# Kernel tuning notes

Hardware: AMD Instinct MI355X
Metric: run time of the kernel (lower is better)

Reference implementation:

```python
import jax, jax.numpy as jnp
import numpy as np

B, T, D, H = 64, 512, 256, 1024


def setup_inputs() -> dict:
    key = jax.random.key(0)
    ks = jax.random.split(key, 4)
    def xavier(k, shape):
        fan_in, fan_out = shape[1], shape[0]
        lim = np.sqrt(6.0 / (fan_in + fan_out)).astype(np.float32)
        return jax.random.uniform(k, shape, jnp.float32, -lim, lim)
    inputs = jax.random.normal(ks[0], (B, T, D), dtype=jnp.float32)
    Wx = xavier(ks[1], (4 * H, D))      # x2h weight
    bx = jnp.zeros((4 * H,), jnp.float32)
    Wh = xavier(ks[2], (4 * H, H))      # h2h weight
    bh = jnp.zeros((4 * H,), jnp.float32)
    Wout = xavier(ks[3], (D, H))        # output head
    bout = jnp.zeros((D,), jnp.float32)
    return {"inputs": inputs, "Wx": Wx, "bx": bx, "Wh": Wh, "bh": bh,
            "Wout": Wout, "bout": bout}


def _lstm_seq(inputs, Wx, bx, Wh, bh):
    # Precompute input-to-hidden gates for all timesteps: (T, B, 4H)
    xg = jnp.einsum('btd,gd->tbg', inputs, Wx) + bx
    h0 = jnp.zeros((inputs.shape[0], H), inputs.dtype)
    c0 = jnp.zeros_like(h0)

    def step(carry, xg_t):
        h, c = carry
        gates = xg_t + h @ Wh.T + bh            # (B, 4H)
        i, f, g, o = jnp.split(jax.nn.sigmoid(gates), 4, axis=-1)
        # NOTE: source applies sigmoid to the cell gate too (not tanh)
        c = c * f + i * g
        h = o * jnp.tanh(c)
        return (h, c), h

    _, hs = jax.lax.scan(step, (h0, c0), xg)    # hs: (T, B, H)
    return jnp.transpose(hs, (1, 0, 2))         # (B, T, H)


def reference(inputs, Wx, bx, Wh, bh, Wout, bout):
    hs = _lstm_seq(inputs, Wx, bx, Wh, bh)      # (B, T, H)
    # Faithful to source: output head uses raw hiddens; returned hidden is tanh'd
    out = jnp.einsum('bth,dh->btd', hs, Wout) + bout
    hidden = jnp.tanh(hs)
    return out, hidden
```

## Files before the change

kernel.cpp:

```cpp
#include <hip/hip_runtime.h>
#include <math.h>

#define BB 64
#define TT 512
#define DD 256
#define HH 1024
#define GG 4096

typedef __bf16 bf16x8 __attribute__((ext_vector_type(8)));
typedef float floatx4 __attribute__((ext_vector_type(4)));

__global__ void cvt_bf16_kernel(const float* __restrict__ src,
                                __bf16* __restrict__ dst, int n) {
    int i = (blockIdx.x * blockDim.x + threadIdx.x) * 8;
    if (i >= n) return;
    float4 a = *(const float4*)(src + i);
    float4 b = *(const float4*)(src + i + 4);
    bf16x8 v;
    v[0] = (__bf16)a.x; v[1] = (__bf16)a.y; v[2] = (__bf16)a.z; v[3] = (__bf16)a.w;
    v[4] = (__bf16)b.x; v[5] = (__bf16)b.y; v[6] = (__bf16)b.z; v[7] = (__bf16)b.w;
    *(bf16x8*)(dst + i) = v;
}

__global__ void init_misc_kernel(const float* __restrict__ bx,
                                 const float* __restrict__ bh,
                                 float* __restrict__ bc,
                                 float* __restrict__ cst) {
    int i = blockIdx.x * blockDim.x + threadIdx.x;
    if (i < GG) bc[i] = bx[i] + bh[i];
    if (i < BB * HH) cst[i] = 0.0f;
}

__global__ __launch_bounds__(256) void lstm_step_kernel(
    const float* __restrict__ x,
    const __bf16* __restrict__ Wxb,
    const __bf16* __restrict__ Whb,
    const float* __restrict__ bc,
    float* __restrict__ cst,
    float* __restrict__ hs,
    __bf16* __restrict__ hping,
    int t) {
    __shared__ __bf16 W_s[16][1288];
    __shared__ float gate_s[64][17];

    const int tid = threadIdx.x;
    const int j0 = blockIdx.x * 4;

    for (int ch = tid; ch < 2560; ch += 256) {
        int r = ch / 160;
        int pos = ch - r * 160;
        int k = pos * 8;
        int gate = r >> 2;
        int jj = r & 3;
        int gr = gate * HH + j0 + jj;
        const __bf16* src = (k < DD) ? (Wxb + (size_t)gr * DD + k)
                                     : (Whb + (size_t)gr * HH + (k - DD));
        *(uint4*)(&W_s[r][k]) = *(const uint4*)src;
    }
    __syncthreads();

    const int wave = tid >> 6;
    const int lane = tid & 63;
    const int ln = lane & 15;
    const int q = lane >> 4;
    const int brow = wave * 16 + ln;

    floatx4 acc = {0.f, 0.f, 0.f, 0.f};

    {
        const float* xrow = x + ((size_t)brow * TT + t) * DD;
#pragma unroll
        for (int k0 = 0; k0 < DD; k0 += 32) {
            int ka = k0 + q * 8;
            float4 f0 = *(const float4*)(xrow + ka);
            float4 f1 = *(const float4*)(xrow + ka + 4);
            bf16x8 av;
            av[0] = (__bf16)f0.x; av[1] = (__bf16)f0.y;
            av[2] = (__bf16)f0.z; av[3] = (__bf16)f0.w;
            av[4] = (__bf16)f1.x; av[5] = (__bf16)f1.y;
            av[6] = (__bf16)f1.z; av[7] = (__bf16)f1.w;
            bf16x8 bv = *(const bf16x8*)(&W_s[ln][ka]);
            acc = __builtin_amdgcn_mfma_f32_16x16x32_bf16(av, bv, acc, 0, 0, 0);
        }
    }

    if (t > 0) {
        const __bf16* hrow =
            hping + (size_t)((t - 1) & 1) * (BB * HH) + (size_t)brow * HH;
#pragma unroll 8
        for (int k0 = 0; k0 < HH; k0 += 32) {
            int ka = k0 + q * 8;
            bf16x8 av = *(const bf16x8*)(hrow + ka);
            bf16x8 bv = *(const bf16x8*)(&W_s[ln][DD + ka]);
            acc = __builtin_amdgcn_mfma_f32_16x16x32_bf16(av, bv, acc, 0, 0, 0);
        }
    }

#pragma unroll
    for (int r = 0; r < 4; ++r)
        gate_s[wave * 16 + q * 4 + r][ln] = acc[r];
    __syncthreads();

    const int b2 = tid >> 2;
    const int jj = tid & 3;
    const int j = j0 + jj;
    float iv = gate_s[b2][jj]      + bc[j];
    float fv = gate_s[b2][4 + jj]  + bc[HH + j];
    float gv = gate_s[b2][8 + jj]  + bc[2 * HH + j];
    float ov = gate_s[b2][12 + jj] + bc[3 * HH + j];
    iv = 1.f / (1.f + expf(-iv));
    fv = 1.f / (1.f + expf(-fv));
    gv = 1.f / (1.f + expf(-gv));
    ov = 1.f / (1.f + expf(-ov));
    float cc = cst[b2 * HH + j];
    cc = cc * fv + iv * gv;
    cst[b2 * HH + j] = cc;
    float hh = ov * tanhf(cc);
    hs[((size_t)b2 * TT + t) * HH + j] = hh;
    hping[(size_t)(t & 1) * (BB * HH) + b2 * HH + j] = (__bf16)hh;
}

__global__ __launch_bounds__(256) void out_gemm_kernel(
    const float* __restrict__ hs,
    const __bf16* __restrict__ Wob,
    const float* __restrict__ bout,
    float* __restrict__ out) {
    __shared__ __bf16 Wout_s[16][1032];
    const int tid = threadIdx.x;
    const int d0 = blockIdx.x * 16;
    const int row0 = blockIdx.y * 64;

    for (int ch = tid; ch < 2048; ch += 256) {
        int r = ch >> 7;
        int k = (ch & 127) * 8;
        *(uint4*)(&Wout_s[r][k]) = *(const uint4*)(Wob + (size_t)(d0 + r) * HH + k);
    }
    __syncthreads();

    const int wave = tid >> 6;
    const int lane = tid & 63;
    const int ln = lane & 15;
    const int q = lane >> 4;
    const int row = row0 + wave * 16 + ln;

    const float* arow = hs + (size_t)row * HH;
    floatx4 acc = {0.f, 0.f, 0.f, 0.f};
#pragma unroll 8
    for (int k0 = 0; k0 < HH; k0 += 32) {
        int ka = k0 + q * 8;
        float4 f0 = *(const float4*)(arow + ka);
        float4 f1 = *(const float4*)(arow + ka + 4);
        bf16x8 av;
        av[0] = (__bf16)f0.x; av[1] = (__bf16)f0.y;
        av[2] = (__bf16)f0.z; av[3] = (__bf16)f0.w;
        av[4] = (__bf16)f1.x; av[5] = (__bf16)f1.y;
        av[6] = (__bf16)f1.z; av[7] = (__bf16)f1.w;
        bf16x8 bv = *(const bf16x8*)(&Wout_s[ln][ka]);
        acc = __builtin_amdgcn_mfma_f32_16x16x32_bf16(av, bv, acc, 0, 0, 0);
    }
    float bo = bout[d0 + ln];
    const int orow0 = row0 + wave * 16 + q * 4;
#pragma unroll
    for (int r = 0; r < 4; ++r)
        out[(size_t)(orow0 + r) * DD + d0 + ln] = acc[r] + bo;
}

__global__ void tanh_inplace_kernel(float* __restrict__ p, size_t n) {
    size_t i = ((size_t)blockIdx.x * blockDim.x + threadIdx.x) * 4;
    size_t stride = (size_t)gridDim.x * blockDim.x * 4;
    for (; i < n; i += stride) {
        float4 v = *(float4*)(p + i);
        v.x = tanhf(v.x); v.y = tanhf(v.y); v.z = tanhf(v.z); v.w = tanhf(v.w);
        *(float4*)(p + i) = v;
    }
}

extern "C" void kernel_launch(void* const* d_in, const int* in_sizes, int n_in,
                              void* d_out, int out_size, void* d_ws, size_t ws_size,
                              hipStream_t stream) {
    const float* x    = (const float*)d_in[0];
    const float* Wx   = (const float*)d_in[1];
    const float* bx   = (const float*)d_in[2];
    const float* Wh   = (const float*)d_in[3];
    const float* bh   = (const float*)d_in[4];
    const float* Wout = (const float*)d_in[5];
    const float* bout = (const float*)d_in[6];

    float* out = (float*)d_out;
    float* hidden = out + (size_t)BB * TT * DD;

    char* ws = (char*)d_ws;
    __bf16* Wxb = (__bf16*)(ws);
    __bf16* Whb = (__bf16*)(ws + (size_t)2 * 1024 * 1024);
    __bf16* Wob = (__bf16*)(ws + (size_t)10 * 1024 * 1024 + 512 * 1024 - 512 * 1024);
    Wob = (__bf16*)(ws + 10485760);
    float* bc   = (float*)(ws + 11010048);
    float* cst  = (float*)(ws + 11026432);
    __bf16* hping = (__bf16*)(ws + 11288576);

    cvt_bf16_kernel<<<(GG * DD / 8 + 255) / 256, 256, 0, stream>>>(Wx, Wxb, GG * DD);
    cvt_bf16_kernel<<<(GG * HH / 8 + 255) / 256, 256, 0, stream>>>(Wh, Whb, GG * HH);
    cvt_bf16_kernel<<<(DD * HH / 8 + 255) / 256, 256, 0, stream>>>(Wout, Wob, DD * HH);
    init_misc_kernel<<<(BB * HH + 255) / 256, 256, 0, stream>>>(bx, bh, bc, cst);

    for (int t = 0; t < TT; ++t) {
        lstm_step_kernel<<<HH / 4, 256, 0, stream>>>(x, Wxb, Whb, bc, cst,
                                                     hidden, hping, t);
    }

    out_gemm_kernel<<<dim3(DD / 16, (BB * TT) / 64), 256, 0, stream>>>(
        hidden, Wob, bout, out);
    tanh_inplace_kernel<<<2048, 256, 0, stream>>>(hidden, (size_t)BB * TT * HH);
}
```

Measured before the change: 6.750 ms.

## Fuse per-timestep LSTM launches into a persistent kernel with grid barrier

Replaces 512 per-timestep kernel launches with one persistent kernel of 256 blocks. Each block keeps its weight slice in shared memory and its cell state in registers for all steps, and synchronises with the other blocks through a striped atomic counter barrier. It also computes the next step's input projection before the barrier so that work overlaps the wait, and swaps sigmoid/tanh for fast exp+rcp versions. Risks include deadlock if all 256 blocks are not co-resident, and a small loss of accuracy from the fast transcendentals.

Measured after the change: 21.32 ms. 3.16x slower.

```diff
diff --git a/kernel.cpp b/kernel.cpp
--- a/kernel.cpp
+++ b/kernel.cpp
@@ -6,9 +6,17 @@
 #define DD 256
 #define HH 1024
 #define GG 4096
+#define NBLK 256
 
 typedef __bf16 bf16x8 __attribute__((ext_vector_type(8)));
 typedef float floatx4 __attribute__((ext_vector_type(4)));
+
+__device__ __forceinline__ float fast_sigmoid(float x) {
+    return __builtin_amdgcn_rcpf(1.0f + __expf(-x));
+}
+__device__ __forceinline__ float fast_tanh(float x) {
+    return 1.0f - 2.0f * __builtin_amdgcn_rcpf(1.0f + __expf(2.0f * x));
+}
 
 __global__ void cvt_bf16_kernel(const float* __restrict__ src,
                                 __bf16* __restrict__ dst, int n) {
@@ -25,21 +33,20 @@
 __global__ void init_misc_kernel(const float* __restrict__ bx,
                                  const float* __restrict__ bh,
                                  float* __restrict__ bc,
-                                 float* __restrict__ cst) {
+                                 int* __restrict__ bar) {
     int i = blockIdx.x * blockDim.x + threadIdx.x;
     if (i < GG) bc[i] = bx[i] + bh[i];
-    if (i < BB * HH) cst[i] = 0.0f;
-}
-
-__global__ __launch_bounds__(256) void lstm_step_kernel(
+    if (i < 256) bar[i] = 0;
+}
+
+__global__ __launch_bounds__(256) void lstm_persist_kernel(
     const float* __restrict__ x,
     const __bf16* __restrict__ Wxb,
     const __bf16* __restrict__ Whb,
     const float* __restrict__ bc,
-    float* __restrict__ cst,
     float* __restrict__ hs,
     __bf16* __restrict__ hping,
-    int t) {
+    int* __restrict__ bar) {
     __shared__ __bf16 W_s[16][1288];
     __shared__ float gate_s[64][17];
 
@@ -51,8 +58,8 @@
         int pos = ch - r * 160;
         int k = pos * 8;
         int gate = r >> 2;
-        int jj = r & 3;
-        int gr = gate * HH + j0 + jj;
+        int jj_ = r & 3;
+        int gr = gate * HH + j0 + jj_;
         const __bf16* src = (k < DD) ? (Wxb + (size_t)gr * DD + k)
                                      : (Whb + (size_t)gr * HH + (k - DD));
         *(uint4*)(&W_s[r][k]) = *(const uint4*)src;
@@ -65,10 +72,21 @@
     const int q = lane >> 4;
     const int brow = wave * 16 + ln;
 
-    floatx4 acc = {0.f, 0.f, 0.f, 0.f};
-
+    const int b2 = tid >> 2;
+    const int jj = tid & 3;
+    const int j = j0 + jj;
+    const float bci = bc[j];
+    const float bcf = bc[HH + j];
+    const float bcg = bc[2 * HH + j];
+    const float bco = bc[3 * HH + j];
+    float creg = 0.0f;
+
+    const float* xbase = x + (size_t)brow * TT * DD;
+    float* hs_pt = hs + (size_t)b2 * TT * HH + j;
+
+    floatx4 acc_x = {0.f, 0.f, 0.f, 0.f};
     {
-        const float* xrow = x + ((size_t)brow * TT + t) * DD;
+        const float* xrow = xbase;
 #pragma unroll
         for (int k0 = 0; k0 < DD; k0 += 32) {
             int ka = k0 + q * 8;
@@ -80,44 +98,75 @@
             av[4] = (__bf16)f1.x; av[5] = (__bf16)f1.y;
             av[6] = (__bf16)f1.z; av[7] = (__bf16)f1.w;
             bf16x8 bv = *(const bf16x8*)(&W_s[ln][ka]);
-            acc = __builtin_amdgcn_mfma_f32_16x16x32_bf16(av, bv, acc, 0, 0, 0);
+            acc_x = __builtin_amdgcn_mfma_f32_16x16x32_bf16(av, bv, acc_x, 0, 0, 0);
         }
     }
 
-    if (t > 0) {
-        const __bf16* hrow =
-            hping + (size_t)((t - 1) & 1) * (BB * HH) + (size_t)brow * HH;
+    int target = 0;
+    for (int t = 0; t < TT; ++t) {
+        floatx4 acc = acc_x;
+
+        if (t > 0) {
+            const __bf16* hrow =
+                hping + (size_t)((t - 1) & 1) * (BB * HH) + (size_t)brow * HH;
 #pragma unroll 8
-        for (int k0 = 0; k0 < HH; k0 += 32) {
-            int ka = k0 + q * 8;
-            bf16x8 av = *(const bf16x8*)(hrow + ka);
-            bf16x8 bv = *(const bf16x8*)(&W_s[ln][DD + ka]);
-            acc = __builtin_amdgcn_mfma_f32_16x16x32_bf16(av, bv, acc, 0, 0, 0);
+            for (int k0 = 0; k0 < HH; k0 += 32) {
+                int ka = k0 + q * 8;
+                bf16x8 av = *(const bf16x8*)(hrow + ka);
+                bf16x8 bv = *(const bf16x8*)(&W_s[ln][DD + ka]);
+                acc = __builtin_amdgcn_mfma_f32_16x16x32_bf16(av, bv, acc, 0, 0, 0);
+            }
         }
-    }
-
-#pragma unroll
-    for (int r = 0; r < 4; ++r)
-        gate_s[wave * 16 + q * 4 + r][ln] = acc[r];
-    __syncthreads();
-
-    const int b2 = tid >> 2;
-    const int jj = tid & 3;
-    const int j = j0 + jj;
-    float iv = gate_s[b2][jj]      + bc[j];
-    float fv = gate_s[b2][4 + jj]  + bc[HH + j];
-    float gv = gate_s[b2][8 + jj]  + bc[2 * HH + j];
-    float ov = gate_s[b2][12 + jj] + bc[3 * HH + j];
-    iv = 1.f / (1.f + expf(-iv));
-    fv = 1.f / (1.f + expf(-fv));
-    gv = 1.f / (1.f + expf(-gv));
-    ov = 1.f / (1.f + expf(-ov));
-    float cc = cst[b2 * HH + j];
-    cc = cc * fv + iv * gv;
-    cst[b2 * HH + j] = cc;
-    float hh = ov * tanhf(cc);
-    hs[((size_t)b2 * TT + t) * HH + j] = hh;
-    hping[(size_t)(t & 1) * (BB * HH) + b2 * HH + j] = (__bf16)hh;
+
+#pragma unroll
+        for (int r = 0; r < 4; ++r)
+            gate_s[wave * 16 + q * 4 + r][ln] = acc[r];
+        __syncthreads();
+
+        float iv = fast_sigmoid(gate_s[b2][jj] + bci);
+        float fv = fast_sigmoid(gate_s[b2][4 + jj] + bcf);
+        float gv = fast_sigmoid(gate_s[b2][8 + jj] + bcg);
+        float ov = fast_sigmoid(gate_s[b2][12 + jj] + bco);
+        creg = creg * fv + iv * gv;
+        float hh = ov * fast_tanh(creg);
+        hs_pt[(size_t)t * HH] = hh;
+        hping[(size_t)(t & 1) * (BB * HH) + b2 * HH + j] = (__bf16)hh;
+
+        if (t + 1 < TT) {
+            const float* xrow = xbase + (size_t)(t + 1) * DD;
+            floatx4 ax = {0.f, 0.f, 0.f, 0.f};
+#pragma unroll
+            for (int k0 = 0; k0 < DD; k0 += 32) {
+                int ka = k0 + q * 8;
+                float4 f0 = *(const float4*)(xrow + ka);
+                float4 f1 = *(const float4*)(xrow + ka + 4);
+                bf16x8 av;
+                av[0] = (__bf16)f0.x; av[1] = (__bf16)f0.y;
+                av[2] = (__bf16)f0.z; av[3] = (__bf16)f0.w;
+                av[4] = (__bf16)f1.x; av[5] = (__bf16)f1.y;
+                av[6] = (__bf16)f1.z; av[7] = (__bf16)f1.w;
+                bf16x8 bv = *(const bf16x8*)(&W_s[ln][ka]);
+                ax = __builtin_amdgcn_mfma_f32_16x16x32_bf16(av, bv, ax, 0, 0, 0);
+            }
+            acc_x = ax;
+
+            target += NBLK;
+            __syncthreads();
+            if (tid == 0) {
+                __hip_atomic_fetch_add(&bar[(blockIdx.x & 7) * 32], 1,
+                                       __ATOMIC_RELEASE, __HIP_MEMORY_SCOPE_AGENT);
+                int sum;
+                do {
+                    sum = 0;
+#pragma unroll
+                    for (int i = 0; i < 8; ++i)
+                        sum += __hip_atomic_load(&bar[i * 32], __ATOMIC_ACQUIRE,
+                                                 __HIP_MEMORY_SCOPE_AGENT);
+                } while (sum < target);
+            }
+            __syncthreads();
+        }
+    }
 }
 
 __global__ __launch_bounds__(256) void out_gemm_kernel(
@@ -170,7 +219,8 @@
     size_t stride = (size_t)gridDim.x * blockDim.x * 4;
     for (; i < n; i += stride) {
         float4 v = *(float4*)(p + i);
-        v.x = tanhf(v.x); v.y = tanhf(v.y); v.z = tanhf(v.z); v.w = tanhf(v.w);
+        v.x = fast_tanh(v.x); v.y = fast_tanh(v.y);
+        v.z = fast_tanh(v.z); v.w = fast_tanh(v.w);
         *(float4*)(p + i) = v;
     }
 }
@@ -190,23 +240,19 @@
     float* hidden = out + (size_t)BB * TT * DD;
 
     char* ws = (char*)d_ws;
-    __bf16* Wxb = (__bf16*)(ws);
-    __bf16* Whb = (__bf16*)(ws + (size_t)2 * 1024 * 1024);
-    __bf16* Wob = (__bf16*)(ws + (size_t)10 * 1024 * 1024 + 512 * 1024 - 512 * 1024);
-    Wob = (__bf16*)(ws + 10485760);
-    float* bc   = (float*)(ws + 11010048);
-    float* cst  = (float*)(ws + 11026432);
-    __bf16* hping = (__bf16*)(ws + 11288576);
+    __bf16* Wxb   = (__bf16*)(ws);
+    __bf16* Whb   = (__bf16*)(ws + 2097152);
+    __bf16* Wob   = (__bf16*)(ws + 10485760);
+    float*  bc    = (float*)(ws + 11010048);
+    __bf16* hping = (__bf16*)(ws + 11026432);
+    int*    bar   = (int*)(ws + 11288576);
 
     cvt_bf16_kernel<<<(GG * DD / 8 + 255) / 256, 256, 0, stream>>>(Wx, Wxb, GG * DD);
     cvt_bf16_kernel<<<(GG * HH / 8 + 255) / 256, 256, 0, stream>>>(Wh, Whb, GG * HH);
     cvt_bf16_kernel<<<(DD * HH / 8 + 255) / 256, 256, 0, stream>>>(Wout, Wob, DD * HH);
-    init_misc_kernel<<<(BB * HH + 255) / 256, 256, 0, stream>>>(bx, bh, bc, cst);
-
-    for (int t = 0; t < TT; ++t) {
-        lstm_step_kernel<<<HH / 4, 256, 0, stream>>>(x, Wxb, Whb, bc, cst,
-                                                     hidden, hping, t);
-    }
+    init_misc_kernel<<<(GG + 255) / 256, 256, 0, stream>>>(bx, bh, bc, bar);
+
+    lstm_persist_kernel<<<NBLK, 256, 0, stream>>>(x, Wxb, Whb, bc, hidden, hping, bar);
 
     out_gemm_kernel<<<dim3(DD / 16, (BB * TT) / 64), 256, 0, stream>>>(
         hidden, Wob, bout, out);
```
